# Kernel tuning notes

Measured on AMD Instinct MI355X. Metric: run time of the kernel, lower is better.

## Reference

```python
import jax, jax.numpy as jnp
import numpy as np


def _gcn(x, src, dst, W, b, n):
    # symmetric normalization: deg computed on edges WITH self-loops (weights 1)
    deg = jax.ops.segment_sum(jnp.ones_like(src, dtype=x.dtype), dst, num_segments=n)
    dinv = jnp.where(deg > 0, jax.lax.rsqrt(deg), 0.0)
    norm = dinv[src] * dinv[dst]              # [E+n]
    xw = x @ W                                # [n, out] transform first (cheaper)
    msg = xw[src] * norm[:, None]             # gather + edge scale
    return jax.ops.segment_sum(msg, dst, num_segments=n) + b


def setup_inputs() -> dict:
    key = jax.random.key(0)
    ks = jax.random.split(key, 8)
    N, E = 100_000, 1_280_000
    x = jax.random.normal(ks[0], (N, 18), dtype=jnp.float32)
    edge_index = jax.random.randint(ks[1], (2, E), 0, N, dtype=jnp.int32)
    W1 = jax.random.normal(ks[2], (18, 32), dtype=jnp.float32) * 0.2
    b1 = jnp.zeros((32,), dtype=jnp.float32)
    W2 = jax.random.normal(ks[3], (32, 64), dtype=jnp.float32) * 0.15
    b2 = jnp.zeros((64,), dtype=jnp.float32)
    Wfc = jax.random.normal(ks[4], (64, 2), dtype=jnp.float32) * 0.1
    bfc = jnp.zeros((2,), dtype=jnp.float32)
    return {"x": x, "edge_index": edge_index, "W1": W1, "b1": b1,
            "W2": W2, "b2": b2, "Wfc": Wfc, "bfc": bfc}


def reference(x, edge_index, W1, b1, W2, b2, Wfc, bfc):
    n = x.shape[0]
    loop = jnp.arange(n, dtype=edge_index.dtype)
    src = jnp.concatenate([edge_index[0], loop])   # add self-loops (PyG default)
    dst = jnp.concatenate([edge_index[1], loop])
    h = jax.nn.relu(_gcn(x, src, dst, W1, b1, n))
    h = jax.nn.relu(_gcn(h, src, dst, W2, b2, n))
    logits = h @ Wfc + bfc
    return jax.nn.log_softmax(logits, axis=1)
```

## Files before the change

### kernel.cpp

```cpp
#include <hip/hip_runtime.h>
#include <hip/hip_fp16.h>
#include <math.h>


#define TPB 256
#define BSH 8
#define BNODES 256
#define MAXBUCK 512
#define CH 8192
#define CAPSH 13
#define CAP (1 << CAPSH)

__global__ void k_part(const int* __restrict__ src, const int* __restrict__ dst,
                       int* __restrict__ bcursor, int* __restrict__ eb,
                       __half* __restrict__ u1h, __half* __restrict__ u2h,
                       int E, int n, int nbuck) {
    __shared__ int lh[MAXBUCK];
    __shared__ int lbase[MAXBUCK];
    int t = threadIdx.x;
    if (blockIdx.x == 0 && t < 32) {
        u1h[(size_t)n * 32 + t] = __float2half_rn(0.f);
        u2h[(size_t)n * 32 + t] = __float2half_rn(0.f);
    }
    int chunk0 = blockIdx.x * CH;
    int end = min(chunk0 + CH, E);
    const int4* dst4 = (const int4*)dst;
    const int4* src4 = (const int4*)src;
    for (int i = t; i < nbuck; i += TPB) lh[i] = 0;
    __syncthreads();
    for (int e4 = chunk0 / 4 + t; e4 * 4 < end; e4 += TPB) {
        int base = e4 * 4;
        int4 d = dst4[e4];
        if (base + 0 < end) atomicAdd(&lh[d.x >> BSH], 1);
        if (base + 1 < end) atomicAdd(&lh[d.y >> BSH], 1);
        if (base + 2 < end) atomicAdd(&lh[d.z >> BSH], 1);
        if (base + 3 < end) atomicAdd(&lh[d.w >> BSH], 1);
    }
    __syncthreads();
    for (int i = t; i < nbuck; i += TPB) {
        int c = lh[i];
        lbase[i] = c ? atomicAdd(&bcursor[i], c) : 0;
        lh[i] = 0;
    }
    __syncthreads();
    for (int e4 = chunk0 / 4 + t; e4 * 4 < end; e4 += TPB) {
        int base = e4 * 4;
        int4 d = dst4[e4];
        int4 s = src4[e4];
        #define PUT(c, sv) if (base + c < end) { \
            int b = (d.sv) >> BSH; \
            int r = lbase[b] + atomicAdd(&lh[b], 1); \
            if (r < CAP) \
                eb[((size_t)b << CAPSH) + r] = ((s.sv) << BSH) | ((d.sv) & (BNODES - 1)); }
        PUT(0, x) PUT(1, y) PUT(2, z) PUT(3, w)
        #undef PUT
    }
}

__global__ void k_bucket(const int* __restrict__ eb, const int* __restrict__ bcursor,
                         const float* __restrict__ x, const float* __restrict__ W1,
                         int* __restrict__ csr, int* __restrict__ row_start,
                         int* __restrict__ cnt4, float* __restrict__ dinv,
                         int* __restrict__ perm,
                         __half* __restrict__ u1h, int n) {
    __shared__ int lcnt[BNODES];
    __shared__ int lscan[BNODES];
    __shared__ float ldinv[BNODES];
    __shared__ int lkey[BNODES];
    __shared__ float xs[BNODES * 18];
    int b = blockIdx.x;
    int t = threadIdx.x;
    int node0 = b << BSH;
    int beg = b << CAPSH;
    int end = beg + min(bcursor[b], CAP);
    lcnt[t] = 0;
    __syncthreads();
    for (int i = beg + t; i < end; i += TPB)
        atomicAdd(&lcnt[eb[i] & (BNODES - 1)], 1);
    __syncthreads();
    int v = lcnt[t];
    int pad = (v + 3) & ~3;
    lscan[t] = pad;
    lkey[t] = (v << 8) | t;
    __syncthreads();
    for (int off = 1; off < TPB; off <<= 1) {
        int xx = (t >= off) ? lscan[t - off] : 0;
        __syncthreads();
        lscan[t] += xx;
        __syncthreads();
    }
    int pexcl = lscan[t] - pad;
    int node = node0 + t;
    float dv = rsqrtf(1.0f + (float)v);
    ldinv[t] = dv;
    if (node < n) {
        row_start[node] = beg + pexcl;
        cnt4[node] = pad >> 2;
        dinv[node] = dv;
    }
    __syncthreads();
    lcnt[t] = pexcl;
    __syncthreads();
    for (int i = beg + t; i < end; i += TPB) {
        int e = eb[i];
        int p = atomicAdd(&lcnt[e & (BNODES - 1)], 1);
        csr[beg + p] = e >> BSH;
    }
    __syncthreads();
    for (int p = v; p < pad; ++p) csr[beg + pexcl + p] = n;
    for (int k = 2; k <= BNODES; k <<= 1) {
        for (int j = k >> 1; j > 0; j >>= 1) {
            int ixj = t ^ j;
            int mine = lkey[t], other = lkey[ixj];
            bool up = ((t & k) == 0);
            int mn = min(mine, other), mx = max(mine, other);
            int keep = ((ixj > t) == up) ? mn : mx;
            __syncthreads();
            lkey[t] = keep;
            __syncthreads();
        }
    }
    perm[node0 + t] = node0 + (lkey[t] & (BNODES - 1));
    int nn = min(BNODES, n - node0);
    const float* xb = x + (size_t)node0 * 18;
    int tot18 = nn * 18;
    for (int i = t; i < tot18; i += TPB) xs[i] = xb[i];
    __syncthreads();
    int f = t & 31, g = t >> 5;
    float w1r[18];
#pragma unroll
    for (int k = 0; k < 18; ++k) w1r[k] = W1[k * 32 + f];
    __half* ub = u1h + (size_t)node0 * 32;
    for (int nl = g; nl < nn; nl += 8) {
        const float* rp = &xs[nl * 18];
        float a = 0.f;
#pragma unroll
        for (int k = 0; k < 18; ++k) a = fmaf(rp[k], w1r[k], a);
        ub[nl * 32 + f] = __float2half_rn(a * ldinv[nl]);
    }
}

__global__ void k_fused1(const uint2* __restrict__ u1q, const int* __restrict__ row_start,
                         const int* __restrict__ cnt4, const int* __restrict__ csr,
                         const float* __restrict__ dinv, const int* __restrict__ perm,
                         const float* __restrict__ b1, __half* __restrict__ u2h,
                         int n) {
    int t = threadIdx.x;
    int lane = t & 63, wv = t >> 6;
    int q = lane & 7, grp = lane >> 3;
    int slot = (blockIdx.x * 4 + wv) * 8 + grp;
    int node = perm[slot];
    if (node >= n) return;
    float4 bb = ((const float4*)b1)[q];
    uint2 sv = u1q[(size_t)node * 8 + q];
    __half2* sh = (__half2*)&sv;
    float2 s01 = __half22float2(sh[0]), s23 = __half22float2(sh[1]);
    float a0 = s01.x, a1 = s01.y, a2 = s23.x, a3 = s23.y;
    int beg = row_start[node];
    int it = cnt4[node];
    const int4* ip = (const int4*)(csr + beg);
    if (it > 0) {
        int4 s = ip[0];
        for (int i = 0; i < it; ++i) {
            int4 nx = ip[i + 1];
            uint2 v0 = u1q[(size_t)s.x * 8 + q];
            uint2 v1 = u1q[(size_t)s.y * 8 + q];
            uint2 v2 = u1q[(size_t)s.z * 8 + q];
            uint2 v3 = u1q[(size_t)s.w * 8 + q];
            __half2* p0 = (__half2*)&v0; __half2* p1 = (__half2*)&v1;
            __half2* p2 = (__half2*)&v2; __half2* p3 = (__half2*)&v3;
            float2 f00 = __half22float2(p0[0]), f01 = __half22float2(p0[1]);
            float2 f10 = __half22float2(p1[0]), f11 = __half22float2(p1[1]);
            float2 f20 = __half22float2(p2[0]), f21 = __half22float2(p2[1]);
            float2 f30 = __half22float2(p3[0]), f31 = __half22float2(p3[1]);
            a0 += (f00.x + f10.x) + (f20.x + f30.x);
            a1 += (f00.y + f10.y) + (f20.y + f30.y);
            a2 += (f01.x + f11.x) + (f21.x + f31.x);
            a3 += (f01.y + f11.y) + (f21.y + f31.y);
            s = nx;
        }
    }
    float di = dinv[node];
    float r0 = fmaxf(fmaf(di, a0, bb.x), 0.f) * di;
    float r1 = fmaxf(fmaf(di, a1, bb.y), 0.f) * di;
    float r2 = fmaxf(fmaf(di, a2, bb.z), 0.f) * di;
    float r3 = fmaxf(fmaf(di, a3, bb.w), 0.f) * di;
    uint2 st;
    __half2* sp = (__half2*)&st;
    sp[0].x = __float2half_rn(r0); sp[0].y = __float2half_rn(r1);
    sp[1].x = __float2half_rn(r2); sp[1].y = __float2half_rn(r3);
    ((uint2*)u2h)[(size_t)node * 8 + q] = st;
}

__global__ void k_fused2(const uint2* __restrict__ u2q, const int* __restrict__ row_start,
                         const int* __restrict__ cnt4, const int* __restrict__ csr,
                         const float* __restrict__ dinv, const int* __restrict__ perm,
                         const float* __restrict__ W2,
                         const float* __restrict__ b2, const float* __restrict__ Wfc,
                         const float* __restrict__ bfc, float* __restrict__ out,
                         int n) {
    __shared__ float lagg[4][8][33];
    int t = threadIdx.x;
    int lane = t & 63, wv = t >> 6;
    int q = lane & 7, grp = lane >> 3;
    float w2r[32];
#pragma unroll
    for (int k = 0; k < 32; ++k) w2r[k] = W2[k * 64 + lane];
    float b2v = b2[lane];
    float wf0 = Wfc[lane * 2 + 0], wf1 = Wfc[lane * 2 + 1];
    float bf0 = bfc[0], bf1 = bfc[1];
    int slot0 = (blockIdx.x * 4 + wv) * 8;
    int node = perm[slot0 + grp];
    float a0 = 0.f, a1 = 0.f, a2 = 0.f, a3 = 0.f;
    if (node < n) {
        uint2 sv = u2q[(size_t)node * 8 + q];
        __half2* sh = (__half2*)&sv;
        float2 s01 = __half22float2(sh[0]), s23 = __half22float2(sh[1]);
        a0 = s01.x; a1 = s01.y; a2 = s23.x; a3 = s23.y;
        int beg = row_start[node];
        int it = cnt4[node];
        const int4* ip = (const int4*)(csr + beg);
        if (it > 0) {
            int4 s = ip[0];
            for (int i = 0; i < it; ++i) {
                int4 nx = ip[i + 1];
                uint2 v0 = u2q[(size_t)s.x * 8 + q];
                uint2 v1 = u2q[(size_t)s.y * 8 + q];
                uint2 v2 = u2q[(size_t)s.z * 8 + q];
                uint2 v3 = u2q[(size_t)s.w * 8 + q];
                __half2* p0 = (__half2*)&v0; __half2* p1 = (__half2*)&v1;
                __half2* p2 = (__half2*)&v2; __half2* p3 = (__half2*)&v3;
                float2 f00 = __half22float2(p0[0]), f01 = __half22float2(p0[1]);
                float2 f10 = __half22float2(p1[0]), f11 = __half22float2(p1[1]);
                float2 f20 = __half22float2(p2[0]), f21 = __half22float2(p2[1]);
                float2 f30 = __half22float2(p3[0]), f31 = __half22float2(p3[1]);
                a0 += (f00.x + f10.x) + (f20.x + f30.x);
                a1 += (f00.y + f10.y) + (f20.y + f30.y);
                a2 += (f01.x + f11.x) + (f21.x + f31.x);
                a3 += (f01.y + f11.y) + (f21.y + f31.y);
                s = nx;
            }
        }
    }
    lagg[wv][grp][4 * q + 0] = a0;
    lagg[wv][grp][4 * q + 1] = a1;
    lagg[wv][grp][4 * q + 2] = a2;
    lagg[wv][grp][4 * q + 3] = a3;
#pragma unroll
    for (int r = 0; r < 8; ++r) {
        int nodeT = perm[slot0 + r];
        const float* rp = lagg[wv][r];
        float c0 = 0.f, c1 = 0.f, c2 = 0.f, c3 = 0.f;
#pragma unroll
        for (int k = 0; k < 32; k += 4) {
            c0 = fmaf(rp[k],     w2r[k],     c0);
            c1 = fmaf(rp[k + 1], w2r[k + 1], c1);
            c2 = fmaf(rp[k + 2], w2r[k + 2], c2);
            c3 = fmaf(rp[k + 3], w2r[k + 3], c3);
        }
        float a = (c0 + c1) + (c2 + c3);
        float v = (nodeT < n) ? fmaxf(fmaf(dinv[nodeT], a, b2v), 0.f) : 0.f;
        float l0 = v * wf0;
        float l1 = v * wf1;
#pragma unroll
        for (int off = 32; off >= 1; off >>= 1) {
            l0 += __shfl_xor(l0, off, 64);
            l1 += __shfl_xor(l1, off, 64);
        }
        if (lane == 0 && nodeT < n) {
            l0 += bf0;
            l1 += bf1;
            float m2 = fmaxf(l0, l1);
            float lse = m2 + logf(expf(l0 - m2) + expf(l1 - m2));
            out[nodeT * 2 + 0] = l0 - lse;
            out[nodeT * 2 + 1] = l1 - lse;
        }
    }
}

extern "C" void kernel_launch(void* const* d_in, const int* in_sizes, int n_in,
                              void* d_out, int out_size, void* d_ws, size_t ws_size,
                              hipStream_t stream) {
    const float* x   = (const float*)d_in[0];
    const int*   ei  = (const int*)d_in[1];
    const float* W1  = (const float*)d_in[2];
    const float* b1  = (const float*)d_in[3];
    const float* W2  = (const float*)d_in[4];
    const float* b2  = (const float*)d_in[5];
    const float* Wfc = (const float*)d_in[6];
    const float* bfc = (const float*)d_in[7];
    float* out = (float*)d_out;

    const int n = in_sizes[0] / 18;
    const int E = in_sizes[1] / 2;
    const int* src = ei;
    const int* dst = ei + E;
    const int nbuck = (n + BNODES - 1) >> BSH;

    char* w = (char*)d_ws;
    int*    bcursor   = (int*)w;     w += (size_t)nbuck * 4;
    int*    row_start = (int*)w;     w += (size_t)n * 4;
    int*    cnt4      = (int*)w;     w += (size_t)n * 4;
    float*  dinv      = (float*)w;   w += (size_t)n * 4;
    int*    perm      = (int*)w;     w += (size_t)nbuck * BNODES * 4;
    int*    eb        = (int*)w;     w += (size_t)nbuck * CAP * 4;
    int*    csr       = (int*)w;     w += (size_t)nbuck * CAP * 4 + 64;
    w = (char*)(((size_t)w + 63) & ~(size_t)63);
    __half* u1h       = (__half*)w;  w += (size_t)(n + 1) * 32 * 2;
    w = (char*)(((size_t)w + 63) & ~(size_t)63);
    __half* u2h       = (__half*)w;  w += (size_t)(n + 1) * 32 * 2;

    hipMemsetAsync(bcursor, 0, (size_t)nbuck * 4, stream);
    k_part<<<(E + CH - 1) / CH, TPB, 0, stream>>>(src, dst, bcursor, eb, u1h, u2h, E, n, nbuck);
    k_bucket<<<nbuck, TPB, 0, stream>>>(eb, bcursor, x, W1, csr, row_start, cnt4,
                                        dinv, perm, u1h, n);

    const int blocksF = nbuck * 8;

    k_fused1<<<blocksF, TPB, 0, stream>>>((const uint2*)u1h, row_start, cnt4, csr,
                                          dinv, perm, b1, u2h, n);
    k_fused2<<<blocksF, TPB, 0, stream>>>((const uint2*)u2h, row_start, cnt4, csr,
                                          dinv, perm, W2, b2, Wfc, bfc, out, n);
}
```

Before: 189.0 us.

## Drop degree-sorted node permutation and gather eight neighbors per iteration

Removes the per-bucket bitonic sort that ordered nodes by degree and the perm indirection in both aggregation kernels, so nodes are processed in natural order. Pads each node's adjacency to a multiple of eight and unrolls the gather loop to issue eight neighbor loads per iteration, meant to increase memory-level parallelism. This trades away load balancing within wavefronts and adds more padded dummy loads per node.

```diff
diff --git a/kernel.cpp b/kernel.cpp
--- a/kernel.cpp
+++ b/kernel.cpp
@@ -60,13 +60,11 @@
 __global__ void k_bucket(const int* __restrict__ eb, const int* __restrict__ bcursor,
                          const float* __restrict__ x, const float* __restrict__ W1,
                          int* __restrict__ csr, int* __restrict__ row_start,
-                         int* __restrict__ cnt4, float* __restrict__ dinv,
-                         int* __restrict__ perm,
+                         int* __restrict__ cnt8, float* __restrict__ dinv,
                          __half* __restrict__ u1h, int n) {
     __shared__ int lcnt[BNODES];
     __shared__ int lscan[BNODES];
     __shared__ float ldinv[BNODES];
-    __shared__ int lkey[BNODES];
     __shared__ float xs[BNODES * 18];
     int b = blockIdx.x;
     int t = threadIdx.x;
@@ -79,9 +77,8 @@
         atomicAdd(&lcnt[eb[i] & (BNODES - 1)], 1);
     __syncthreads();
     int v = lcnt[t];
-    int pad = (v + 3) & ~3;
+    int pad = (v + 7) & ~7;
     lscan[t] = pad;
-    lkey[t] = (v << 8) | t;
     __syncthreads();
     for (int off = 1; off < TPB; off <<= 1) {
         int xx = (t >= off) ? lscan[t - off] : 0;
@@ -95,7 +92,7 @@
     ldinv[t] = dv;
     if (node < n) {
         row_start[node] = beg + pexcl;
-        cnt4[node] = pad >> 2;
+        cnt8[node] = pad >> 3;
         dinv[node] = dv;
     }
     __syncthreads();
@@ -108,19 +105,6 @@
     }
     __syncthreads();
     for (int p = v; p < pad; ++p) csr[beg + pexcl + p] = n;
-    for (int k = 2; k <= BNODES; k <<= 1) {
-        for (int j = k >> 1; j > 0; j >>= 1) {
-            int ixj = t ^ j;
-            int mine = lkey[t], other = lkey[ixj];
-            bool up = ((t & k) == 0);
-            int mn = min(mine, other), mx = max(mine, other);
-            int keep = ((ixj > t) == up) ? mn : mx;
-            __syncthreads();
-            lkey[t] = keep;
-            __syncthreads();
-        }
-    }
-    perm[node0 + t] = node0 + (lkey[t] & (BNODES - 1));
     int nn = min(BNODES, n - node0);
     const float* xb = x + (size_t)node0 * 18;
     int tot18 = nn * 18;
@@ -140,44 +124,55 @@
     }
 }
 
+#define CVT4(vv, r0, r1, r2, r3) \
+    { __half2* _p = (__half2*)&(vv); \
+      float2 _fl = __half22float2(_p[0]), _fh = __half22float2(_p[1]); \
+      r0 = _fl.x; r1 = _fl.y; r2 = _fh.x; r3 = _fh.y; }
+
+#define GATHER8(uq, sA, sB, q, a0, a1, a2, a3) \
+    { uint2 _v0 = uq[(size_t)(sA).x * 8 + (q)]; \
+      uint2 _v1 = uq[(size_t)(sA).y * 8 + (q)]; \
+      uint2 _v2 = uq[(size_t)(sA).z * 8 + (q)]; \
+      uint2 _v3 = uq[(size_t)(sA).w * 8 + (q)]; \
+      uint2 _v4 = uq[(size_t)(sB).x * 8 + (q)]; \
+      uint2 _v5 = uq[(size_t)(sB).y * 8 + (q)]; \
+      uint2 _v6 = uq[(size_t)(sB).z * 8 + (q)]; \
+      uint2 _v7 = uq[(size_t)(sB).w * 8 + (q)]; \
+      float _x0,_y0,_z0,_w0, _x1,_y1,_z1,_w1, _x2,_y2,_z2,_w2, _x3,_y3,_z3,_w3; \
+      float _x4,_y4,_z4,_w4, _x5,_y5,_z5,_w5, _x6,_y6,_z6,_w6, _x7,_y7,_z7,_w7; \
+      CVT4(_v0,_x0,_y0,_z0,_w0) CVT4(_v1,_x1,_y1,_z1,_w1) \
+      CVT4(_v2,_x2,_y2,_z2,_w2) CVT4(_v3,_x3,_y3,_z3,_w3) \
+      CVT4(_v4,_x4,_y4,_z4,_w4) CVT4(_v5,_x5,_y5,_z5,_w5) \
+      CVT4(_v6,_x6,_y6,_z6,_w6) CVT4(_v7,_x7,_y7,_z7,_w7) \
+      a0 += ((_x0+_x1)+(_x2+_x3)) + ((_x4+_x5)+(_x6+_x7)); \
+      a1 += ((_y0+_y1)+(_y2+_y3)) + ((_y4+_y5)+(_y6+_y7)); \
+      a2 += ((_z0+_z1)+(_z2+_z3)) + ((_z4+_z5)+(_z6+_z7)); \
+      a3 += ((_w0+_w1)+(_w2+_w3)) + ((_w4+_w5)+(_w6+_w7)); }
+
 __global__ void k_fused1(const uint2* __restrict__ u1q, const int* __restrict__ row_start,
-                         const int* __restrict__ cnt4, const int* __restrict__ csr,
-                         const float* __restrict__ dinv, const int* __restrict__ perm,
+                         const int* __restrict__ cnt8, const int* __restrict__ csr,
+                         const float* __restrict__ dinv,
                          const float* __restrict__ b1, __half* __restrict__ u2h,
                          int n) {
     int t = threadIdx.x;
     int lane = t & 63, wv = t >> 6;
     int q = lane & 7, grp = lane >> 3;
-    int slot = (blockIdx.x * 4 + wv) * 8 + grp;
-    int node = perm[slot];
+    int node = (blockIdx.x * 4 + wv) * 8 + grp;
     if (node >= n) return;
     float4 bb = ((const float4*)b1)[q];
     uint2 sv = u1q[(size_t)node * 8 + q];
-    __half2* sh = (__half2*)&sv;
-    float2 s01 = __half22float2(sh[0]), s23 = __half22float2(sh[1]);
-    float a0 = s01.x, a1 = s01.y, a2 = s23.x, a3 = s23.y;
+    float a0, a1, a2, a3;
+    CVT4(sv, a0, a1, a2, a3)
     int beg = row_start[node];
-    int it = cnt4[node];
+    int it = cnt8[node];
     const int4* ip = (const int4*)(csr + beg);
     if (it > 0) {
-        int4 s = ip[0];
+        int4 sA = ip[0], sB = ip[1];
         for (int i = 0; i < it; ++i) {
-            int4 nx = ip[i + 1];
-            uint2 v0 = u1q[(size_t)s.x * 8 + q];
-            uint2 v1 = u1q[(size_t)s.y * 8 + q];
-            uint2 v2 = u1q[(size_t)s.z * 8 + q];
-            uint2 v3 = u1q[(size_t)s.w * 8 + q];
-            __half2* p0 = (__half2*)&v0; __half2* p1 = (__half2*)&v1;
-            __half2* p2 = (__half2*)&v2; __half2* p3 = (__half2*)&v3;
-            float2 f00 = __half22float2(p0[0]), f01 = __half22float2(p0[1]);
-            float2 f10 = __half22float2(p1[0]), f11 = __half22float2(p1[1]);
-            float2 f20 = __half22float2(p2[0]), f21 = __half22float2(p2[1]);
-            float2 f30 = __half22float2(p3[0]), f31 = __half22float2(p3[1]);
-            a0 += (f00.x + f10.x) + (f20.x + f30.x);
-            a1 += (f00.y + f10.y) + (f20.y + f30.y);
-            a2 += (f01.x + f11.x) + (f21.x + f31.x);
-            a3 += (f01.y + f11.y) + (f21.y + f31.y);
-            s = nx;
+            int4 nA = ip[2 * i + 2];
+            int4 nB = ip[2 * i + 3];
+            GATHER8(u1q, sA, sB, q, a0, a1, a2, a3)
+            sA = nA; sB = nB;
         }
     }
     float di = dinv[node];
@@ -193,8 +188,8 @@
 }
 
 __global__ void k_fused2(const uint2* __restrict__ u2q, const int* __restrict__ row_start,
-                         const int* __restrict__ cnt4, const int* __restrict__ csr,
-                         const float* __restrict__ dinv, const int* __restrict__ perm,
+                         const int* __restrict__ cnt8, const int* __restrict__ csr,
+                         const float* __restrict__ dinv,
                          const float* __restrict__ W2,
                          const float* __restrict__ b2, const float* __restrict__ Wfc,
                          const float* __restrict__ bfc, float* __restrict__ out,
@@ -209,36 +204,24 @@
     float b2v = b2[lane];
     float wf0 = Wfc[lane * 2 + 0], wf1 = Wfc[lane * 2 + 1];
     float bf0 = bfc[0], bf1 = bfc[1];
-    int slot0 = (blockIdx.x * 4 + wv) * 8;
-    int node = perm[slot0 + grp];
+    int node0 = (blockIdx.x * 4 + wv) * 8;
+    int node = node0 + grp;
     float a0 = 0.f, a1 = 0.f, a2 = 0.f, a3 = 0.f;
     if (node < n) {
         uint2 sv = u2q[(size_t)node * 8 + q];
-        __half2* sh = (__half2*)&sv;
-        float2 s01 = __half22float2(sh[0]), s23 = __half22float2(sh[1]);
-        a0 = s01.x; a1 = s01.y; a2 = s23.x; a3 = s23.y;
+        float s0, s1, s2, s3;
+        CVT4(sv, s0, s1, s2, s3)
+        a0 = s0; a1 = s1; a2 = s2; a3 = s3;
         int beg = row_start[node];
-        int it = cnt4[node];
+        int it = cnt8[node];
         const int4* ip = (const int4*)(csr + beg);
         if (it > 0) {
-            int4 s = ip[0];
+            int4 sA = ip[0], sB = ip[1];
             for (int i = 0; i < it; ++i) {
-                int4 nx = ip[i + 1];
-                uint2 v0 = u2q[(size_t)s.x * 8 + q];
-                uint2 v1 = u2q[(size_t)s.y * 8 + q];
-                uint2 v2 = u2q[(size_t)s.z * 8 + q];
-                uint2 v3 = u2q[(size_t)s.w * 8 + q];
-                __half2* p0 = (__half2*)&v0; __half2* p1 = (__half2*)&v1;
-                __half2* p2 = (__half2*)&v2; __half2* p3 = (__half2*)&v3;
-                float2 f00 = __half22float2(p0[0]), f01 = __half22float2(p0[1]);
-                float2 f10 = __half22float2(p1[0]), f11 = __half22float2(p1[1]);
-                float2 f20 = __half22float2(p2[0]), f21 = __half22float2(p2[1]);
-                float2 f30 = __half22float2(p3[0]), f31 = __half22float2(p3[1]);
-                a0 += (f00.x + f10.x) + (f20.x + f30.x);
-                a1 += (f00.y + f10.y) + (f20.y + f30.y);
-                a2 += (f01.x + f11.x) + (f21.x + f31.x);
-                a3 += (f01.y + f11.y) + (f21.y + f31.y);
-                s = nx;
+                int4 nA = ip[2 * i + 2];
+                int4 nB = ip[2 * i + 3];
+                GATHER8(u2q, sA, sB, q, a0, a1, a2, a3)
+                sA = nA; sB = nB;
             }
         }
     }
@@ -248,7 +231,7 @@
     lagg[wv][grp][4 * q + 3] = a3;
 #pragma unroll
     for (int r = 0; r < 8; ++r) {
-        int nodeT = perm[slot0 + r];
+        int nodeT = node0 + r;
         const float* rp = lagg[wv][r];
         float c0 = 0.f, c1 = 0.f, c2 = 0.f, c3 = 0.f;
 #pragma unroll
@@ -300,9 +283,8 @@
     char* w = (char*)d_ws;
     int*    bcursor   = (int*)w;     w += (size_t)nbuck * 4;
     int*    row_start = (int*)w;     w += (size_t)n * 4;
-    int*    cnt4      = (int*)w;     w += (size_t)n * 4;
+    int*    cnt8      = (int*)w;     w += (size_t)n * 4;
     float*  dinv      = (float*)w;   w += (size_t)n * 4;
-    int*    perm      = (int*)w;     w += (size_t)nbuck * BNODES * 4;
     int*    eb        = (int*)w;     w += (size_t)nbuck * CAP * 4;
     int*    csr       = (int*)w;     w += (size_t)nbuck * CAP * 4 + 64;
     w = (char*)(((size_t)w + 63) & ~(size_t)63);
@@ -312,13 +294,14 @@
 
     hipMemsetAsync(bcursor, 0, (size_t)nbuck * 4, stream);
     k_part<<<(E + CH - 1) / CH, TPB, 0, stream>>>(src, dst, bcursor, eb, u1h, u2h, E, n, nbuck);
-    k_bucket<<<nbuck, TPB, 0, stream>>>(eb, bcursor, x, W1, csr, row_start, cnt4,
-                                        dinv, perm, u1h, n);
-
-    const int blocksF = nbuck * 8;
-
-    k_fused1<<<blocksF, TPB, 0, stream>>>((const uint2*)u1h, row_start, cnt4, csr,
-                                          dinv, perm, b1, u2h, n);
-    k_fused2<<<blocksF, TPB, 0, stream>>>((const uint2*)u2h, row_start, cnt4, csr,
-                                          dinv, perm, W2, b2, Wfc, bfc, out, n);
-}
+    k_bucket<<<nbuck, TPB, 0, stream>>>(eb, bcursor, x, W1, csr, row_start, cnt8,
+                                        dinv, u1h, n);
+
+    const int waves = (n + 7) / 8;
+    const int blocksF = (waves + 3) / 4;
+
+    k_fused1<<<blocksF, TPB, 0, stream>>>((const uint2*)u1h, row_start, cnt8, csr,
+                                          dinv, b1, u2h, n);
+    k_fused2<<<blocksF, TPB, 0, stream>>>((const uint2*)u2h, row_start, cnt8, csr,
+                                          dinv, W2, b2, Wfc, bfc, out, n);
+}
```

New measurement: 172.3 us. -8.9%, faster.
